# Kernel tuning notes

Measured on AMD Instinct MI355X. Metric: run time of the kernel, lower is better.

## Reference

```python
import jax, jax.numpy as jnp
import numpy as np

N = 100000          # number of nodes (queries == sources here)
DEG = 32            # uniform neighbor count
E = N * DEG         # total edges
C_IN = 8
HID = 32
C_OUT = 32


def setup_inputs() -> dict:
    key = jax.random.key(0)
    k1, k2, k3, k4, k5 = jax.random.split(key, 5)
    in_features = jax.random.normal(k1, (N, C_IN), dtype=jnp.float32)
    in_weights = jax.random.uniform(k2, (N,), dtype=jnp.float32)
    # MLP: Linear(2*C_IN -> HID), GELU, Linear(HID -> C_OUT)
    W1 = jax.random.normal(k3, (2 * C_IN, HID), dtype=jnp.float32) / np.sqrt(2 * C_IN)
    b1 = jnp.zeros((HID,), dtype=jnp.float32)
    W2 = jax.random.normal(k4, (HID, C_OUT), dtype=jnp.float32) / np.sqrt(HID)
    b2 = jnp.zeros((C_OUT,), dtype=jnp.float32)
    neighbor_index = jax.random.randint(k5, (E,), 0, N, dtype=jnp.int64)
    row_splits = (jnp.arange(N + 1, dtype=jnp.int64) * DEG)  # uniform CSR splits
    return {"in_features": in_features, "in_weights": in_weights,
            "W1": W1, "b1": b1, "W2": W2, "b2": b2,
            "neighbor_index": neighbor_index, "row_splits": row_splits}


def reference(in_features, in_weights, W1, b1, W2, b2, neighbor_index, row_splits):
    num_edges = neighbor_index.shape[0]
    num_out = row_splits.shape[0] - 1  # M output nodes
    # segment id of each edge (== repeat_interleave of node ids by row counts)
    seg = jnp.searchsorted(row_splits, jnp.arange(num_edges), side="right") - 1
    gathered = in_features[neighbor_index]          # [E, C_in] neighbor gather
    self_feats = in_features[seg]                   # [E, C_in] repeated self features
    agg = jnp.concatenate([gathered, self_feats], axis=1)  # [E, 2*C_in]
    h = jax.nn.gelu(agg @ W1 + b1)                  # [E, HID]
    h = h @ W2 + b2                                 # [E, C_out]
    h = in_weights[neighbor_index][:, None] * h     # quadrature weighting
    sums = jax.ops.segment_sum(h, seg, num_segments=num_out)  # segment_csr sum
    counts = (row_splits[1:] - row_splits[:-1]).astype(h.dtype)
    out = sums / jnp.maximum(counts, 1)[:, None]    # reduce='mean'
    return out
```

## Files before the change

kernel.cpp:

```cpp
#include <hip/hip_runtime.h>

#define DEG 32
#define HID 32
#define CIN 8

__device__ __forceinline__ float gelu_tanh(float x) {
    constexpr float A = (float)(2.0 * 1.4426950408889634 * 0.7978845608028654);
    constexpr float B = (float)(2.0 * 1.4426950408889634 * 0.7978845608028654 * 0.044715);
    float x2 = x * x;
    float z  = x * fmaf(B, x2, A);
    float e  = __builtin_amdgcn_exp2f(z);
    float r  = __builtin_amdgcn_rcpf(1.0f + e);
    return fmaf(-x, r, x);
}

__global__ __launch_bounds__(256) void precompute_u(
    const float* __restrict__ x, const float* __restrict__ W1,
    float* __restrict__ u, int N) {
    int tid = blockIdx.x * 256 + threadIdx.x;
    if (tid >= N * (HID / 4)) return;
    int n  = tid >> 3;
    int hq = tid & 7;
    const float4* xp = (const float4*)(x + (size_t)n * CIN);
    float4 a = xp[0], b = xp[1];
    float xv[8] = {a.x, a.y, a.z, a.w, b.x, b.y, b.z, b.w};
    float4 s = make_float4(0.f, 0.f, 0.f, 0.f);
#pragma unroll
    for (int k = 0; k < 8; ++k) {
        float4 wrow = *(const float4*)(W1 + k * HID + hq * 4);
        s.x = fmaf(xv[k], wrow.x, s.x);
        s.y = fmaf(xv[k], wrow.y, s.y);
        s.z = fmaf(xv[k], wrow.z, s.z);
        s.w = fmaf(xv[k], wrow.w, s.w);
    }
    *(float4*)(u + (size_t)n * HID + hq * 4) = s;
}

__global__ __launch_bounds__(256) void git_main(
    const float* __restrict__ u, const float* __restrict__ x,
    const float* __restrict__ wgt, const float* __restrict__ W1,
    const float* __restrict__ b1, const float* __restrict__ W2,
    const float* __restrict__ b2, const int* __restrict__ nbr,
    float* __restrict__ out, int N) {
    __shared__ float sW2[HID * HID];
    __shared__ float sb2[HID];
    __shared__ int2  sp[8 * DEG];

    int t = threadIdx.x;
#pragma unroll
    for (int i = 0; i < 4; ++i) sW2[t + i * 256] = W2[t + i * 256];
    if (t < HID) sb2[t] = b2[t];

    int slot = t >> 5;
    int hid  = t & 31;
    int node = blockIdx.x * 8 + slot;
    bool valid = node < N;
    int nc = valid ? node : (N - 1);

    int   j_own = nbr[nc * DEG + hid];
    float w_own = wgt[j_own];
    sp[slot * DEG + hid] = make_int2(j_own * (HID * 4), __float_as_int(w_own));

    const float4* xip = (const float4*)(x + (size_t)nc * CIN);
    float4 xa = xip[0], xb = xip[1];
    float vb = b1[hid];
    vb = fmaf(xa.x, W1[ 8 * HID + hid], vb);
    vb = fmaf(xa.y, W1[ 9 * HID + hid], vb);
    vb = fmaf(xa.z, W1[10 * HID + hid], vb);
    vb = fmaf(xa.w, W1[11 * HID + hid], vb);
    vb = fmaf(xb.x, W1[12 * HID + hid], vb);
    vb = fmaf(xb.y, W1[13 * HID + hid], vb);
    vb = fmaf(xb.z, W1[14 * HID + hid], vb);
    vb = fmaf(xb.w, W1[15 * HID + hid], vb);

    float ws = w_own;
    ws += __shfl_xor(ws, 1);
    ws += __shfl_xor(ws, 2);
    ws += __shfl_xor(ws, 4);
    ws += __shfl_xor(ws, 8);
    ws += __shfl_xor(ws, 16);

    __syncthreads();

    const char* ub = (const char*)u;
    const int2* myp = &sp[slot * DEG];
    int hid4 = hid * 4;
    float g = 0.f;
#pragma unroll
    for (int e = 0; e < DEG; ++e) {
        int2  p  = myp[e];
        float uj = *(const float*)(ub + (unsigned)(p.x + hid4));
        g = fmaf(__int_as_float(p.y), gelu_tanh(uj + vb), g);
    }

    float acc = 0.f;
#pragma unroll
    for (int h = 0; h < HID; ++h) {
        float gh = __shfl(g, h, 32);
        acc = fmaf(gh, sW2[h * HID + hid], acc);
    }
    if (valid) {
        out[(size_t)node * HID + hid] = fmaf(ws, sb2[hid], acc) * (1.0f / DEG);
    }
}

__global__ __launch_bounds__(256) void fused_fallback(
    const float* __restrict__ x, const float* __restrict__ wgt,
    const float* __restrict__ W1, const float* __restrict__ b1,
    const float* __restrict__ W2, const float* __restrict__ b2,
    const int* __restrict__ nbr, float* __restrict__ out, int N) {
    __shared__ float sW2[HID * HID];
    __shared__ float sb2[HID];
    __shared__ int2  sp[8 * DEG];
    int t = threadIdx.x;
#pragma unroll
    for (int i = 0; i < 4; ++i) sW2[t + i * 256] = W2[t + i * 256];
    if (t < HID) sb2[t] = b2[t];
    int slot = t >> 5, hid = t & 31;
    int node = blockIdx.x * 8 + slot;
    bool valid = node < N;
    int nc = valid ? node : (N - 1);
    int   j_own = nbr[nc * DEG + hid];
    float w_own = wgt[j_own];
    sp[slot * DEG + hid] = make_int2(j_own * (CIN * 4), __float_as_int(w_own));
    const float4* xip = (const float4*)(x + (size_t)nc * CIN);
    float4 xa = xip[0], xb = xip[1];
    float w1t[8];
#pragma unroll
    for (int k = 0; k < 8; ++k) w1t[k] = W1[k * HID + hid];
    float vb = b1[hid];
    vb = fmaf(xa.x, W1[ 8 * HID + hid], vb);
    vb = fmaf(xa.y, W1[ 9 * HID + hid], vb);
    vb = fmaf(xa.z, W1[10 * HID + hid], vb);
    vb = fmaf(xa.w, W1[11 * HID + hid], vb);
    vb = fmaf(xb.x, W1[12 * HID + hid], vb);
    vb = fmaf(xb.y, W1[13 * HID + hid], vb);
    vb = fmaf(xb.z, W1[14 * HID + hid], vb);
    vb = fmaf(xb.w, W1[15 * HID + hid], vb);
    float ws = w_own;
    ws += __shfl_xor(ws, 1);  ws += __shfl_xor(ws, 2);
    ws += __shfl_xor(ws, 4);  ws += __shfl_xor(ws, 8);
    ws += __shfl_xor(ws, 16);
    __syncthreads();
    const char* xbytes = (const char*)x;
    const int2* myp = &sp[slot * DEG];
    float g = 0.f;
#pragma unroll 8
    for (int e = 0; e < DEG; ++e) {
        int2  p  = myp[e];
        float wj = __int_as_float(p.y);
        const float4* xjp = (const float4*)(xbytes + (unsigned)p.x);
        float4 a = xjp[0], b = xjp[1];
        float tin = vb;
        tin = fmaf(a.x, w1t[0], tin); tin = fmaf(a.y, w1t[1], tin);
        tin = fmaf(a.z, w1t[2], tin); tin = fmaf(a.w, w1t[3], tin);
        tin = fmaf(b.x, w1t[4], tin); tin = fmaf(b.y, w1t[5], tin);
        tin = fmaf(b.z, w1t[6], tin); tin = fmaf(b.w, w1t[7], tin);
        g = fmaf(wj, gelu_tanh(tin), g);
    }
    float acc = 0.f;
#pragma unroll
    for (int h = 0; h < HID; ++h) {
        float gh = __shfl(g, h, 32);
        acc = fmaf(gh, sW2[h * HID + hid], acc);
    }
    if (valid) out[(size_t)node * HID + hid] = fmaf(ws, sb2[hid], acc) * (1.0f / DEG);
}

extern "C" void kernel_launch(void* const* d_in, const int* in_sizes, int n_in,
                              void* d_out, int out_size, void* d_ws, size_t ws_size,
                              hipStream_t stream) {
    const float* x   = (const float*)d_in[0];
    const float* wq  = (const float*)d_in[1];
    const float* W1  = (const float*)d_in[2];
    const float* b1  = (const float*)d_in[3];
    const float* W2  = (const float*)d_in[4];
    const float* b2  = (const float*)d_in[5];
    const int*   nbr = (const int*)d_in[6];
    float* out = (float*)d_out;

    int N = in_sizes[1];
    size_t need = (size_t)N * HID * sizeof(float);
    int blocks_main = (N + 7) / 8;

    if (ws_size >= need) {
        float* u = (float*)d_ws;
        int threads_pre = N * (HID / 4);
        int blocks_pre = (threads_pre + 255) / 256;
        precompute_u<<<blocks_pre, 256, 0, stream>>>(x, W1, u, N);
        git_main<<<blocks_main, 256, 0, stream>>>(u, x, wq, W1, b1, W2, b2, nbr, out, N);
    } else {
        fused_fallback<<<blocks_main, 256, 0, stream>>>(x, wq, W1, b1, W2, b2, nbr, out, N);
    }
}
```

Before: 135.2 us.

## Store precomputed hidden projection in bf16 and restructure main kernel per wavefront

The precomputed per-node W1 projection is now stored as packed bf16 with round-to-nearest, halving the random-gather footprint from 128 to 64 bytes per node. The main kernel maps one 64-lane wavefront per node, with each lane handling two hidden channels over eight edges. It uses packed float2 math and cross-lane shuffles in place of a shared-memory index table. This cuts gather bandwidth and shortens the per-thread edge loop, at the cost of bf16 rounding error in the pre-activation and extra shuffle reductions.

```diff
diff --git a/kernel.cpp b/kernel.cpp
--- a/kernel.cpp
+++ b/kernel.cpp
@@ -4,103 +4,140 @@
 #define HID 32
 #define CIN 8
 
-__device__ __forceinline__ float gelu_tanh(float x) {
-    constexpr float A = (float)(2.0 * 1.4426950408889634 * 0.7978845608028654);
-    constexpr float B = (float)(2.0 * 1.4426950408889634 * 0.7978845608028654 * 0.044715);
-    float x2 = x * x;
-    float z  = x * fmaf(B, x2, A);
-    float e  = __builtin_amdgcn_exp2f(z);
-    float r  = __builtin_amdgcn_rcpf(1.0f + e);
-    return fmaf(-x, r, x);
-}
-
-__global__ __launch_bounds__(256) void precompute_u(
+typedef float v2f __attribute__((ext_vector_type(2)));
+
+#define GELU_A ((float)(2.0 * 1.4426950408889634 * 0.7978845608028654))
+#define GELU_B ((float)(2.0 * 1.4426950408889634 * 0.7978845608028654 * 0.044715))
+
+__device__ __forceinline__ unsigned f2bf(float f) {
+    unsigned b = __float_as_uint(f);
+    return (b + 0x7fffu + ((b >> 16) & 1u)) >> 16;
+}
+
+__global__ __launch_bounds__(256) void precompute_u16(
     const float* __restrict__ x, const float* __restrict__ W1,
-    float* __restrict__ u, int N) {
+    unsigned* __restrict__ u16, int N) {
     int tid = blockIdx.x * 256 + threadIdx.x;
-    if (tid >= N * (HID / 4)) return;
-    int n  = tid >> 3;
-    int hq = tid & 7;
+    if (tid >= N * 4) return;
+    int n = tid >> 2;
+    int q = tid & 3;
     const float4* xp = (const float4*)(x + (size_t)n * CIN);
     float4 a = xp[0], b = xp[1];
     float xv[8] = {a.x, a.y, a.z, a.w, b.x, b.y, b.z, b.w};
-    float4 s = make_float4(0.f, 0.f, 0.f, 0.f);
+    float s[8];
+#pragma unroll
+    for (int c = 0; c < 8; ++c) s[c] = 0.f;
 #pragma unroll
     for (int k = 0; k < 8; ++k) {
-        float4 wrow = *(const float4*)(W1 + k * HID + hq * 4);
-        s.x = fmaf(xv[k], wrow.x, s.x);
-        s.y = fmaf(xv[k], wrow.y, s.y);
-        s.z = fmaf(xv[k], wrow.z, s.z);
-        s.w = fmaf(xv[k], wrow.w, s.w);
-    }
-    *(float4*)(u + (size_t)n * HID + hq * 4) = s;
-}
-
-__global__ __launch_bounds__(256) void git_main(
-    const float* __restrict__ u, const float* __restrict__ x,
+        float4 w0 = *(const float4*)(W1 + k * HID + q * 8);
+        float4 w1 = *(const float4*)(W1 + k * HID + q * 8 + 4);
+        s[0] = fmaf(xv[k], w0.x, s[0]); s[1] = fmaf(xv[k], w0.y, s[1]);
+        s[2] = fmaf(xv[k], w0.z, s[2]); s[3] = fmaf(xv[k], w0.w, s[3]);
+        s[4] = fmaf(xv[k], w1.x, s[4]); s[5] = fmaf(xv[k], w1.y, s[5]);
+        s[6] = fmaf(xv[k], w1.z, s[6]); s[7] = fmaf(xv[k], w1.w, s[7]);
+    }
+    uint4 o;
+    o.x = f2bf(s[0]) | (f2bf(s[1]) << 16);
+    o.y = f2bf(s[2]) | (f2bf(s[3]) << 16);
+    o.z = f2bf(s[4]) | (f2bf(s[5]) << 16);
+    o.w = f2bf(s[6]) | (f2bf(s[7]) << 16);
+    *(uint4*)(u16 + (size_t)n * 16 + q * 4) = o;
+}
+
+__global__ __launch_bounds__(256, 8) void git_main2(
+    const unsigned* __restrict__ u16, const float* __restrict__ x,
     const float* __restrict__ wgt, const float* __restrict__ W1,
     const float* __restrict__ b1, const float* __restrict__ W2,
     const float* __restrict__ b2, const int* __restrict__ nbr,
     float* __restrict__ out, int N) {
     __shared__ float sW2[HID * HID];
     __shared__ float sb2[HID];
-    __shared__ int2  sp[8 * DEG];
 
     int t = threadIdx.x;
 #pragma unroll
     for (int i = 0; i < 4; ++i) sW2[t + i * 256] = W2[t + i * 256];
     if (t < HID) sb2[t] = b2[t];
-
-    int slot = t >> 5;
-    int hid  = t & 31;
-    int node = blockIdx.x * 8 + slot;
+    __syncthreads();
+
+    int lane = t & 63;
+    int c2   = lane & 15;
+    int eg   = lane >> 4;
+    int node = blockIdx.x * 4 + (t >> 6);
     bool valid = node < N;
     int nc = valid ? node : (N - 1);
 
-    int   j_own = nbr[nc * DEG + hid];
+    int   j_own = nbr[nc * DEG + (lane & 31)];
+    int   off_l = j_own << 6;
     float w_own = wgt[j_own];
-    sp[slot * DEG + hid] = make_int2(j_own * (HID * 4), __float_as_int(w_own));
+
+    float ws = w_own;
+    ws += __shfl_xor(ws, 1);  ws += __shfl_xor(ws, 2);
+    ws += __shfl_xor(ws, 4);  ws += __shfl_xor(ws, 8);
+    ws += __shfl_xor(ws, 16);
 
     const float4* xip = (const float4*)(x + (size_t)nc * CIN);
     float4 xa = xip[0], xb = xip[1];
-    float vb = b1[hid];
-    vb = fmaf(xa.x, W1[ 8 * HID + hid], vb);
-    vb = fmaf(xa.y, W1[ 9 * HID + hid], vb);
-    vb = fmaf(xa.z, W1[10 * HID + hid], vb);
-    vb = fmaf(xa.w, W1[11 * HID + hid], vb);
-    vb = fmaf(xb.x, W1[12 * HID + hid], vb);
-    vb = fmaf(xb.y, W1[13 * HID + hid], vb);
-    vb = fmaf(xb.z, W1[14 * HID + hid], vb);
-    vb = fmaf(xb.w, W1[15 * HID + hid], vb);
-
-    float ws = w_own;
-    ws += __shfl_xor(ws, 1);
-    ws += __shfl_xor(ws, 2);
-    ws += __shfl_xor(ws, 4);
-    ws += __shfl_xor(ws, 8);
-    ws += __shfl_xor(ws, 16);
-
-    __syncthreads();
-
-    const char* ub = (const char*)u;
-    const int2* myp = &sp[slot * DEG];
-    int hid4 = hid * 4;
-    float g = 0.f;
-#pragma unroll
-    for (int e = 0; e < DEG; ++e) {
-        int2  p  = myp[e];
-        float uj = *(const float*)(ub + (unsigned)(p.x + hid4));
-        g = fmaf(__int_as_float(p.y), gelu_tanh(uj + vb), g);
-    }
-
-    float acc = 0.f;
-#pragma unroll
-    for (int h = 0; h < HID; ++h) {
-        float gh = __shfl(g, h, 32);
-        acc = fmaf(gh, sW2[h * HID + hid], acc);
-    }
-    if (valid) {
-        out[(size_t)node * HID + hid] = fmaf(ws, sb2[hid], acc) * (1.0f / DEG);
+    float xs[8] = {xa.x, xa.y, xa.z, xa.w, xb.x, xb.y, xb.z, xb.w};
+    v2f vb = *(const v2f*)(b1 + c2 * 2);
+#pragma unroll
+    for (int k = 0; k < 8; ++k) {
+        v2f wcol = *(const v2f*)(W1 + (8 + k) * HID + c2 * 2);
+        vb += xs[k] * wcol;
+    }
+
+    const char* ub = (const char*)u16;
+    unsigned bits[8];
+    float    wes[8];
+#pragma unroll
+    for (int it = 0; it < 8; ++it) {
+        int src = eg * 8 + it;
+        int off_e = __shfl(off_l, src);
+        wes[it]   = __shfl(w_own, src);
+        bits[it]  = *(const unsigned*)(ub + (unsigned)(off_e + c2 * 4));
+    }
+
+    const v2f As = {GELU_A, GELU_B};
+    v2f g = {0.f, 0.f};
+#pragma unroll
+    for (int it = 0; it < 8; ++it) {
+        unsigned bb = bits[it];
+        v2f uf;
+        uf.x = __uint_as_float(bb << 16);
+        uf.y = __uint_as_float(bb & 0xffff0000u);
+        v2f tt = uf + vb;
+        v2f x2 = tt * tt;
+        v2f zz = tt * (x2 * As.y + As.x);
+        v2f ee;
+        ee.x = __builtin_amdgcn_exp2f(zz.x);
+        ee.y = __builtin_amdgcn_exp2f(zz.y);
+        v2f dd = ee + 1.0f;
+        v2f rr;
+        rr.x = __builtin_amdgcn_rcpf(dd.x);
+        rr.y = __builtin_amdgcn_rcpf(dd.y);
+        v2f gl = tt - tt * rr;
+        v2f we = {wes[it], wes[it]};
+        g += we * gl;
+    }
+
+    g.x += __shfl_xor(g.x, 16);  g.y += __shfl_xor(g.y, 16);
+    g.x += __shfl_xor(g.x, 32);  g.y += __shfl_xor(g.y, 32);
+
+    v2f acc = {0.f, 0.f};
+#pragma unroll
+    for (int hh = 0; hh < 8; ++hh) {
+        int h = eg * 8 + hh;
+        float gh = (hh & 1) ? __shfl(g.y, eg * 4 + (hh >> 1))
+                            : __shfl(g.x, eg * 4 + (hh >> 1));
+        v2f wrow = *(const v2f*)(sW2 + h * HID + c2 * 2);
+        acc += gh * wrow;
+    }
+    acc.x += __shfl_xor(acc.x, 16);  acc.y += __shfl_xor(acc.y, 16);
+    acc.x += __shfl_xor(acc.x, 32);  acc.y += __shfl_xor(acc.y, 32);
+
+    if (valid && eg == 0) {
+        v2f bb2 = *(const v2f*)(sb2 + c2 * 2);
+        v2f res = (acc + ws * bb2) * (1.0f / DEG);
+        *(v2f*)(out + (size_t)node * HID + c2 * 2) = res;
     }
 }
 
@@ -156,7 +193,11 @@
         tin = fmaf(a.z, w1t[2], tin); tin = fmaf(a.w, w1t[3], tin);
         tin = fmaf(b.x, w1t[4], tin); tin = fmaf(b.y, w1t[5], tin);
         tin = fmaf(b.z, w1t[6], tin); tin = fmaf(b.w, w1t[7], tin);
-        g = fmaf(wj, gelu_tanh(tin), g);
+        float x2 = tin * tin;
+        float z  = tin * fmaf(GELU_B, x2, GELU_A);
+        float e2 = __builtin_amdgcn_exp2f(z);
+        float r  = __builtin_amdgcn_rcpf(1.0f + e2);
+        g = fmaf(wj, fmaf(-tin, r, tin), g);
     }
     float acc = 0.f;
 #pragma unroll
@@ -180,16 +221,16 @@
     float* out = (float*)d_out;
 
     int N = in_sizes[1];
-    size_t need = (size_t)N * HID * sizeof(float);
-    int blocks_main = (N + 7) / 8;
+    size_t need = (size_t)N * 64;
 
     if (ws_size >= need) {
-        float* u = (float*)d_ws;
-        int threads_pre = N * (HID / 4);
-        int blocks_pre = (threads_pre + 255) / 256;
-        precompute_u<<<blocks_pre, 256, 0, stream>>>(x, W1, u, N);
-        git_main<<<blocks_main, 256, 0, stream>>>(u, x, wq, W1, b1, W2, b2, nbr, out, N);
+        unsigned* u16 = (unsigned*)d_ws;
+        int blocks_pre = (N * 4 + 255) / 256;
+        precompute_u16<<<blocks_pre, 256, 0, stream>>>(x, W1, u16, N);
+        int blocks_main = (N + 3) / 4;
+        git_main2<<<blocks_main, 256, 0, stream>>>(u16, x, wq, W1, b1, W2, b2, nbr, out, N);
     } else {
-        fused_fallback<<<blocks_main, 256, 0, stream>>>(x, wq, W1, b1, W2, b2, nbr, out, N);
-    }
-}
+        int blocks = (N + 7) / 8;
+        fused_fallback<<<blocks, 256, 0, stream>>>(x, wq, W1, b1, W2, b2, nbr, out, N);
+    }
+}
```

New measurement: 146.0 us. 8.0% more time.
